# Performance work log

Hardware: AMD Instinct MI355X
Metric: run time of the kernel (lower is better)

Reference implementation:

```python
import jax, jax.numpy as jnp
import numpy as np

B, S, H, D = 4, 4096, 8, 128
EPS = 1e-6


def layernorm(x, g, b, axes):
    m = jnp.mean(x, axis=axes, keepdims=True)
    v = jnp.mean(jnp.square(x - m), axis=axes, keepdims=True)
    return (x - m) / jnp.sqrt(v + EPS) * g + b


def setup_inputs() -> dict:
    key = jax.random.key(0)
    ks = jax.random.split(key, 6)
    scale = 0.05
    return {
        "heads_input": jax.random.normal(ks[0], (B, S, H, D), jnp.float32),
        # GroupLinear trans_hid: per-head (2D -> 3D)
        "W_hid": jax.random.normal(ks[1], (H, 2 * D, 3 * D), jnp.float32) * scale,
        "b_hid": jax.random.normal(ks[2], (H, 3 * D), jnp.float32) * scale,
        # GroupLinear trans_og: per-head (2D -> D)
        "W_og": jax.random.normal(ks[3], (H, 2 * D, D), jnp.float32) * scale,
        "b_og": jax.random.normal(ks[4], (H, D), jnp.float32) * scale,
        # LayerNorm affine params (elementwise_affine=True)
        "ln_csum_g": jnp.ones((H, D), jnp.float32),
        "ln_csum_b": jnp.zeros((H, D), jnp.float32),
        "ln_hid_g": jnp.ones((H, 3, D), jnp.float32),
        "ln_hid_b": jnp.zeros((H, 3, D), jnp.float32),
        "ln_og_g": jnp.ones((H, D), jnp.float32),
        "ln_og_b": jnp.zeros((H, D), jnp.float32),
        "init_cx": jnp.zeros((1, H, D), jnp.float32),
    }


def reference(heads_input, W_hid, b_hid, W_og, b_og, ln_csum_g, ln_csum_b,
              ln_hid_g, ln_hid_b, ln_og_g, ln_og_b, init_cx):
    b, s, h, d = heads_input.shape
    # shifted cumulative sum over time, then LayerNorm over (head, dim)
    shifted = jnp.concatenate(
        [jnp.zeros((b, 1, h, d), heads_input.dtype), heads_input[:, :-1]], axis=1)
    csum = layernorm(jnp.cumsum(shifted, axis=1), ln_csum_g, ln_csum_b, (-2, -1))
    cat = jnp.concatenate([heads_input, csum], axis=-1)        # [b,s,h,2d]
    hid = jnp.einsum('bshi,hio->bsho', cat, W_hid) + b_hid     # [b,s,h,3d]
    hid = layernorm(hid.reshape(b, s, h, 3, d), ln_hid_g, ln_hid_b, (-3, -2, -1))
    igate, fgate, hidden = hid[..., 0, :], hid[..., 1, :], hid[..., 2, :]
    fgate = jax.nn.sigmoid(fgate)
    igh = jax.nn.sigmoid(igate) * jax.nn.relu(hidden)
    # LGateFunc: cell_t = fgate_t * cell_{t-1} + igh_t, cell_0 = init_cx
    c0 = jnp.broadcast_to(init_cx, (b, h, d)).astype(heads_input.dtype)
    def step(c, fi):
        f, i = fi
        c = f * c + i
        return c, c
    _, cells = jax.lax.scan(step, c0,
                            (fgate.transpose(1, 0, 2, 3), igh.transpose(1, 0, 2, 3)))
    cell = cells.transpose(1, 0, 2, 3)                          # [b,s,h,d]
    og_in = jnp.concatenate([heads_input, cell], axis=-1)       # [b,s,h,2d]
    og = layernorm(jnp.einsum('bshi,hio->bsho', og_in, W_og) + b_og,
                   ln_og_g, ln_og_b, (-2, -1))
    return jax.nn.sigmoid(og) * cell
```

## Files before the change

### kernel.cpp

```cpp
#include <hip/hip_runtime.h>

#define EPSF 1e-6f


typedef __attribute__((ext_vector_type(8))) short short8v;
typedef __attribute__((ext_vector_type(4))) float float4v;

__device__ __forceinline__ float sigm(float x) { return 1.0f / (1.0f + __expf(-x)); }

__device__ __forceinline__ unsigned short f2bf(float f) {
    unsigned int u = __float_as_uint(f);
    u = (u + 0x7fffu + ((u >> 16) & 1u)) >> 16;
    return (unsigned short)u;
}
__device__ __forceinline__ float bf2f(unsigned short s) { return __uint_as_float(((unsigned int)s) << 16); }
__device__ __forceinline__ float bf2f_lo(unsigned int p) { return __uint_as_float(p << 16); }
__device__ __forceinline__ float bf2f_hi(unsigned int p) { return __uint_as_float(p & 0xffff0000u); }
__device__ __forceinline__ unsigned int pack2bf(float a, float b) {
    return (unsigned int)f2bf(a) | ((unsigned int)f2bf(b) << 16);
}

__device__ __forceinline__ void block_reduce2(float& a, float& b) {
#pragma unroll
    for (int off = 32; off > 0; off >>= 1) {
        a += __shfl_down(a, off);
        b += __shfl_down(b, off);
    }
    __shared__ float sa[8], sb[8];
    int wid = threadIdx.x >> 6;
    int lane = threadIdx.x & 63;
    if (lane == 0) { sa[wid] = a; sb[wid] = b; }
    __syncthreads();
    a = sa[0] + sa[1] + sa[2] + sa[3];
    b = sb[0] + sb[1] + sb[2] + sb[3];
}

__global__ __launch_bounds__(256) void k_prep_w(const float* __restrict__ W, unsigned short* __restrict__ Wt,
                                                int Nw) {
    int idx = blockIdx.x * 256 + threadIdx.x;
    int k = idx & 255;
    int rest = idx >> 8;
    int o = rest % Nw;
    int h = rest / Nw;
    Wt[idx] = f2bf(W[((size_t)h * 256 + k) * Nw + o]);
}

__global__ __launch_bounds__(256) void k_cumsum_a(const float* __restrict__ X, float* __restrict__ cS,
                                                  unsigned short* __restrict__ XB) {
    int t = blockIdx.x * 256 + threadIdx.x;
    int d = t & 127, h = (t >> 7) & 7, k = (t >> 10) & 63, b = t >> 16;
    size_t base = (((size_t)(b * 4096 + k * 64)) * 8 + h) * 128 + d;
    float s = 0.f;
    for (int j = 0; j < 64; ++j) {
        unsigned short xb = f2bf(X[base + (size_t)j * 1024]);
        XB[base + (size_t)j * 1024] = xb;
        s += bf2f(xb);
    }
    cS[(size_t)((b * 8 + h) * 128 + d) * 64 + k] = s;
}

__global__ __launch_bounds__(256) void k_cumsum_b(const float* __restrict__ cS, float* __restrict__ cO) {
    int ch = blockIdx.x * 256 + threadIdx.x;
    size_t base = (size_t)ch * 64;
    float off = 0.f;
    for (int k = 0; k < 64; ++k) { float v = cS[base + k]; cO[base + k] = off; off += v; }
}

__global__ __launch_bounds__(256) void k_cumsum_c(const unsigned short* __restrict__ XB,
                                                  const float* __restrict__ cO,
                                                  unsigned short* __restrict__ CSUMB) {
    int t = blockIdx.x * 256 + threadIdx.x;
    int d = t & 127, h = (t >> 7) & 7, k = (t >> 10) & 63, b = t >> 16;
    int ch = (b * 8 + h) * 128 + d;
    float run = cO[(size_t)ch * 64 + k];
    size_t base = (((size_t)(b * 4096 + k * 64)) * 8 + h) * 128 + d;
    for (int j = 0; j < 64; ++j) {
        float x = bf2f(XB[base + (size_t)j * 1024]);
        CSUMB[base + (size_t)j * 1024] = f2bf(run);
        run += x;
    }
}

__global__ __launch_bounds__(256) void k_ln_csum(const unsigned short* __restrict__ CSUMB,
                                                 unsigned short* __restrict__ CSB,
                                                 const float* __restrict__ g, const float* __restrict__ bb) {
    int bs = blockIdx.x, t = threadIdx.x;
    uint2 u = ((const uint2*)(CSUMB + (size_t)bs * 1024))[t];
    float4 v;
    v.x = bf2f_lo(u.x); v.y = bf2f_hi(u.x);
    v.z = bf2f_lo(u.y); v.w = bf2f_hi(u.y);
    float s = v.x + v.y + v.z + v.w;
    float ss = v.x * v.x + v.y * v.y + v.z * v.z + v.w * v.w;
    block_reduce2(s, ss);
    float m = s * (1.f / 1024.f);
    float var = ss * (1.f / 1024.f) - m * m;
    float r = rsqrtf(fmaxf(var, 0.f) + EPSF);
    float4 gv = ((const float4*)g)[t];
    float4 bv = ((const float4*)bb)[t];
    uint2 o;
    o.x = pack2bf((v.x - m) * r * gv.x + bv.x, (v.y - m) * r * gv.y + bv.y);
    o.y = pack2bf((v.z - m) * r * gv.z + bv.z, (v.w - m) * r * gv.w + bv.w);
    ((uint2*)(CSB + (size_t)bs * 1024))[t] = o;
}

__global__ __launch_bounds__(256) void k_gemm_bf16(const unsigned short* __restrict__ A1,
                                                   const unsigned short* __restrict__ A2,
                                                   const unsigned short* __restrict__ Wt,
                                                   const float* __restrict__ bias,
                                                   unsigned short* __restrict__ OUT, int Nw, int m0) {
    __shared__ short As[16384];
    __shared__ short Bs[16384];
    int h = blockIdx.z, by = blockIdx.y, bx = blockIdx.x;
    int t = threadIdx.x;
    int lane = t & 63, wid = t >> 6;
    int wr = wid >> 1, wc = wid & 1;
    int l15 = lane & 15, l4 = lane >> 4;
    float4v acc[4][4];
#pragma unroll
    for (int i = 0; i < 4; ++i)
#pragma unroll
        for (int j = 0; j < 4; ++j) acc[i][j] = (float4v)(0.f);

    const size_t mbase = (size_t)(m0 + by * 128);
    for (int ks = 0; ks < 2; ++ks) {
        const unsigned short* Asrc = ks ? A2 : A1;
#pragma unroll
        for (int it = 0; it < 8; ++it) {
            int r0 = wid * 32 + it * 4;
            int r = r0 + l4;
            size_t g = ((mbase + r) * 8 + h) * 128 + 8 * (l15 ^ (r & 7));
            __builtin_amdgcn_global_load_lds((const __attribute__((address_space(1))) void*)(Asrc + g),
                                             (__attribute__((address_space(3))) void*)(As + r0 * 128),
                                             16, 0, 0);
        }
#pragma unroll
        for (int it = 0; it < 8; ++it) {
            int n0 = wid * 32 + it * 4;
            int nl = n0 + l4;
            size_t g = ((size_t)(h * Nw + bx * 128 + nl)) * 256 + ks * 128 + 8 * (l15 ^ (nl & 7));
            __builtin_amdgcn_global_load_lds((const __attribute__((address_space(1))) void*)(Wt + g),
                                             (__attribute__((address_space(3))) void*)(Bs + n0 * 128),
                                             16, 0, 0);
        }
        asm volatile("s_waitcnt vmcnt(0)" ::: "memory");
        __syncthreads();
#pragma unroll
        for (int kk = 0; kk < 4; ++kk) {
            short8v a[4], b[4];
#pragma unroll
            for (int i = 0; i < 4; ++i) {
                int r = wr * 64 + i * 16 + l15;
                int slot = (kk * 4 + l4) ^ (r & 7);
                a[i] = *(const short8v*)(As + r * 128 + slot * 8);
            }
#pragma unroll
            for (int j = 0; j < 4; ++j) {
                int c = wc * 64 + j * 16 + l15;
                int slot = (kk * 4 + l4) ^ (c & 7);
                b[j] = *(const short8v*)(Bs + c * 128 + slot * 8);
            }
#pragma unroll
            for (int i = 0; i < 4; ++i)
#pragma unroll
                for (int j = 0; j < 4; ++j)
                    acc[i][j] = __builtin_amdgcn_mfma_f32_16x16x32_bf16(a[i], b[j], acc[i][j], 0, 0, 0);
        }
        __syncthreads();
    }
#pragma unroll
    for (int j = 0; j < 4; ++j) {
        int o = bx * 128 + wc * 64 + j * 16 + l15;
        float bv = bias[h * Nw + o];
#pragma unroll
        for (int i = 0; i < 4; ++i) {
            int mlb = by * 128 + wr * 64 + i * 16 + l4 * 4;
#pragma unroll
            for (int q = 0; q < 4; ++q) {
                OUT[((size_t)(mlb + q) * 8 + h) * Nw + o] = f2bf(acc[i][j][q] + bv);
            }
        }
    }
}

__global__ __launch_bounds__(256) void k_ln_gates(const unsigned short* __restrict__ HID,
                                                  unsigned short* __restrict__ FG,
                                                  unsigned short* __restrict__ IG,
                                                  const float* __restrict__ g, const float* __restrict__ bb,
                                                  int m0) {
    __shared__ float sm[3072];
    int bsl = blockIdx.x, t = threadIdx.x;
    int bs = m0 + bsl;
    const uint4* row = (const uint4*)(HID + (size_t)bsl * 3072);
    float s = 0.f, ss = 0.f;
    for (int idx = t; idx < 384; idx += 256) {
        uint4 u = row[idx];
        float f0 = bf2f_lo(u.x), f1 = bf2f_hi(u.x);
        float f2 = bf2f_lo(u.y), f3 = bf2f_hi(u.y);
        float f4 = bf2f_lo(u.z), f5 = bf2f_hi(u.z);
        float f6 = bf2f_lo(u.w), f7 = bf2f_hi(u.w);
        float* p = sm + idx * 8;
        p[0] = f0; p[1] = f1; p[2] = f2; p[3] = f3; p[4] = f4; p[5] = f5; p[6] = f6; p[7] = f7;
        s += f0 + f1 + f2 + f3 + f4 + f5 + f6 + f7;
        ss += f0 * f0 + f1 * f1 + f2 * f2 + f3 * f3 + f4 * f4 + f5 * f5 + f6 * f6 + f7 * f7;
    }
    block_reduce2(s, ss);
    float m = s * (1.f / 3072.f);
    float var = ss * (1.f / 3072.f) - m * m;
    float r = rsqrtf(fmaxf(var, 0.f) + EPSF);
    int u0 = t * 4;
    int h = u0 >> 7;
    int d0 = u0 & 127;
    float fr[4], ir[4];
#pragma unroll
    for (int q = 0; q < 4; ++q) {
        int d = d0 + q;
        float yi = sm[h * 384 + d];
        float yf = sm[h * 384 + 128 + d];
        float yh = sm[h * 384 + 256 + d];
        float ni = (yi - m) * r * g[(h * 3 + 0) * 128 + d] + bb[(h * 3 + 0) * 128 + d];
        float nf = (yf - m) * r * g[(h * 3 + 1) * 128 + d] + bb[(h * 3 + 1) * 128 + d];
        float nh = (yh - m) * r * g[(h * 3 + 2) * 128 + d] + bb[(h * 3 + 2) * 128 + d];
        fr[q] = sigm(nf);
        ir[q] = sigm(ni) * fmaxf(nh, 0.f);
    }
    uint2 fo, io;
    fo.x = pack2bf(fr[0], fr[1]); fo.y = pack2bf(fr[2], fr[3]);
    io.x = pack2bf(ir[0], ir[1]); io.y = pack2bf(ir[2], ir[3]);
    ((uint2*)(FG + (size_t)bs * 1024))[t] = fo;
    ((uint2*)(IG + (size_t)bs * 1024))[t] = io;
}

__global__ __launch_bounds__(256) void k_scan_a(const unsigned short* __restrict__ FG,
                                                const unsigned short* __restrict__ IG,
                                                float* __restrict__ cF, float* __restrict__ cC) {
    int t = blockIdx.x * 256 + threadIdx.x;
    int d2 = t & 63, h = (t >> 6) & 7, k = (t >> 9) & 63, b = t >> 15;
    size_t base = (((size_t)(b * 4096 + k * 64)) * 8 + h) * 64 + d2;
    const unsigned int* FGu = (const unsigned int*)FG;
    const unsigned int* IGu = (const unsigned int*)IG;
    float F0 = 1.f, C0 = 0.f, F1 = 1.f, C1 = 0.f;
    for (int j = 0; j < 64; ++j) {
        unsigned int fg = FGu[base + (size_t)j * 512];
        unsigned int ig = IGu[base + (size_t)j * 512];
        float f0 = bf2f_lo(fg), f1 = bf2f_hi(fg);
        C0 = fmaf(f0, C0, bf2f_lo(ig)); F0 *= f0;
        C1 = fmaf(f1, C1, bf2f_hi(ig)); F1 *= f1;
    }
    size_t ci0 = ((size_t)((b * 8 + h) * 128 + d2 * 2)) * 64 + k;
    cF[ci0] = F0; cC[ci0] = C0;
    cF[ci0 + 64] = F1; cC[ci0 + 64] = C1;
}

__global__ __launch_bounds__(256) void k_scan_b(const float* __restrict__ cF, const float* __restrict__ cC,
                                                const float* __restrict__ initcx, float* __restrict__ cI) {
    int ch = blockIdx.x * 256 + threadIdx.x;
    float c = initcx[ch & 1023];
    size_t base = (size_t)ch * 64;
    for (int k = 0; k < 64; ++k) {
        cI[base + k] = c;
        c = fmaf(cF[base + k], c, cC[base + k]);
    }
}

__global__ __launch_bounds__(256) void k_scan_c(const unsigned short* __restrict__ FG,
                                                unsigned short* __restrict__ IGCLB,
                                                const float* __restrict__ cI) {
    int t = blockIdx.x * 256 + threadIdx.x;
    int d2 = t & 63, h = (t >> 6) & 7, k = (t >> 9) & 63, b = t >> 15;
    size_t base = (((size_t)(b * 4096 + k * 64)) * 8 + h) * 64 + d2;
    const unsigned int* FGu = (const unsigned int*)FG;
    unsigned int* IGu = (unsigned int*)IGCLB;
    size_t ci0 = ((size_t)((b * 8 + h) * 128 + d2 * 2)) * 64 + k;
    float c0 = cI[ci0], c1 = cI[ci0 + 64];
    for (int j = 0; j < 64; ++j) {
        unsigned int fg = FGu[base + (size_t)j * 512];
        unsigned int ig = IGu[base + (size_t)j * 512];
        c0 = fmaf(bf2f_lo(fg), c0, bf2f_lo(ig));
        c1 = fmaf(bf2f_hi(fg), c1, bf2f_hi(ig));
        IGu[base + (size_t)j * 512] = pack2bf(c0, c1);
    }
}

__global__ __launch_bounds__(256) void k_ln_out(const unsigned short* __restrict__ OG,
                                                const unsigned short* __restrict__ CLB,
                                                const float* __restrict__ g, const float* __restrict__ bb,
                                                float* __restrict__ OUT, int m0) {
    int bsl = blockIdx.x, t = threadIdx.x;
    int bs = m0 + bsl;
    uint2 u = ((const uint2*)(OG + (size_t)bsl * 1024))[t];
    float4 v;
    v.x = bf2f_lo(u.x); v.y = bf2f_hi(u.x);
    v.z = bf2f_lo(u.y); v.w = bf2f_hi(u.y);
    float s = v.x + v.y + v.z + v.w;
    float ss = v.x * v.x + v.y * v.y + v.z * v.z + v.w * v.w;
    block_reduce2(s, ss);
    float m = s * (1.f / 1024.f);
    float var = ss * (1.f / 1024.f) - m * m;
    float r = rsqrtf(fmaxf(var, 0.f) + EPSF);
    float4 gv = ((const float4*)g)[t];
    float4 bv = ((const float4*)bb)[t];
    uint2 cu = ((const uint2*)(CLB + (size_t)bs * 1024))[t];
    float4 cv;
    cv.x = bf2f_lo(cu.x); cv.y = bf2f_hi(cu.x);
    cv.z = bf2f_lo(cu.y); cv.w = bf2f_hi(cu.y);
    float4 o;
    o.x = sigm((v.x - m) * r * gv.x + bv.x) * cv.x;
    o.y = sigm((v.y - m) * r * gv.y + bv.y) * cv.y;
    o.z = sigm((v.z - m) * r * gv.z + bv.z) * cv.z;
    o.w = sigm((v.w - m) * r * gv.w + bv.w) * cv.w;
    ((float4*)(OUT + (size_t)bs * 1024))[t] = o;
}

extern "C" void kernel_launch(void* const* d_in, const int* in_sizes, int n_in,
                              void* d_out, int out_size, void* d_ws, size_t ws_size,
                              hipStream_t stream) {
    const float* X      = (const float*)d_in[0];
    const float* W_hid  = (const float*)d_in[1];
    const float* b_hid  = (const float*)d_in[2];
    const float* W_og   = (const float*)d_in[3];
    const float* b_og   = (const float*)d_in[4];
    const float* g_cs   = (const float*)d_in[5];
    const float* b_cs   = (const float*)d_in[6];
    const float* g_hid  = (const float*)d_in[7];
    const float* b_hidl = (const float*)d_in[8];
    const float* g_og   = (const float*)d_in[9];
    const float* b_ogl  = (const float*)d_in[10];
    const float* initcx = (const float*)d_in[11];

    float* ws = (float*)d_ws;
    const size_t O_SC    = 0ull;
    const size_t O_XB    = 1310720ull;
    const size_t O_CSUMB = 9699328ull;
    const size_t O_CSB   = 18087936ull;
    const size_t O_IGB   = 26476544ull;
    const size_t O_WTH   = 34865152ull;
    const size_t O_WTO   = 35258368ull;
    const size_t O_HID   = 35389440ull;

    float* cS = ws + O_SC;
    float* cO = cS + 262144;
    float* cF = cO + 262144;
    float* cC = cF + 262144;
    float* cI = cC + 262144;
    unsigned short* XB    = (unsigned short*)(ws + O_XB);
    unsigned short* CSUMB = (unsigned short*)(ws + O_CSUMB);
    unsigned short* FGB   = CSUMB;
    unsigned short* CSB   = (unsigned short*)(ws + O_CSB);
    unsigned short* IGB   = (unsigned short*)(ws + O_IGB);
    unsigned short* CLB   = IGB;
    unsigned short* WTH   = (unsigned short*)(ws + O_WTH);
    unsigned short* WTO   = (unsigned short*)(ws + O_WTO);
    unsigned short* HIDC  = (unsigned short*)(ws + O_HID);

    size_t avail = (ws_size / 4 > O_HID) ? ws_size / 4 - O_HID : 0;
    int CH = 1024;
    for (int c = 16384; c >= 1024; c >>= 1) {
        if ((size_t)c * 1536ull <= avail) { CH = c; break; }
    }
    const int NC = 16384 / CH;

    dim3 blk(256);
    k_prep_w<<<3072, blk, 0, stream>>>(W_hid, WTH, 384);
    k_prep_w<<<1024, blk, 0, stream>>>(W_og, WTO, 128);
    k_cumsum_a<<<1024, blk, 0, stream>>>(X, cS, XB);
    k_cumsum_b<<<16, blk, 0, stream>>>(cS, cO);
    k_cumsum_c<<<1024, blk, 0, stream>>>(XB, cO, CSUMB);
    k_ln_csum<<<16384, blk, 0, stream>>>(CSUMB, CSB, g_cs, b_cs);
    for (int c = 0; c < NC; ++c) {
        int m0 = c * CH;
        k_gemm_bf16<<<dim3(3, CH / 128, 8), blk, 0, stream>>>(XB, CSB, WTH, b_hid, HIDC, 384, m0);
        k_ln_gates<<<CH, blk, 0, stream>>>(HIDC, FGB, IGB, g_hid, b_hidl, m0);
    }
    k_scan_a<<<512, blk, 0, stream>>>(FGB, IGB, cF, cC);
    k_scan_b<<<16, blk, 0, stream>>>(cF, cC, initcx, cI);
    k_scan_c<<<512, blk, 0, stream>>>(FGB, IGB, cI);
    for (int c = 0; c < NC; ++c) {
        int m0 = c * CH;
        k_gemm_bf16<<<dim3(1, CH / 128, 8), blk, 0, stream>>>(XB, CLB, WTO, b_og, HIDC, 128, m0);
        k_ln_out<<<CH, blk, 0, stream>>>(HIDC, CLB, g_og, b_ogl, (float*)d_out, m0);
    }
}
```

Baseline: 257.5 us.

## Double-buffer GEMM K-tiles in LDS and remap grid with head-fastest block order

The bf16 GEMM now splits the K dimension into four 64-wide stages and double-buffers them in LDS, so the next stage's global-to-LDS load overlaps the MFMA work on the current one, using partial vmcnt waits and raw barriers. The launch grid is flattened to 1D with the head index fastest, so adjacent blocks work on different heads of the same rows. This keeps the same LDS footprint but adds more barriers and finer-grained stages, and it relies on the vmcnt(8) count matching the number of loads issued per stage.

```diff
diff --git a/kernel.cpp b/kernel.cpp
--- a/kernel.cpp
+++ b/kernel.cpp
@@ -107,57 +107,77 @@
                                                    const unsigned short* __restrict__ A2,
                                                    const unsigned short* __restrict__ Wt,
                                                    const float* __restrict__ bias,
-                                                   unsigned short* __restrict__ OUT, int Nw, int m0) {
-    __shared__ short As[16384];
-    __shared__ short Bs[16384];
-    int h = blockIdx.z, by = blockIdx.y, bx = blockIdx.x;
-    int t = threadIdx.x;
-    int lane = t & 63, wid = t >> 6;
+                                                   unsigned short* __restrict__ OUT, int Nw, int m0,
+                                                   int nbx) {
+    __shared__ short As[2][8192];
+    __shared__ short Bs[2][8192];
+    int bid = blockIdx.x;
+    int h = bid & 7;
+    int rest = bid >> 3;
+    int bx = rest % nbx;
+    int by = rest / nbx;
+    int t0 = threadIdx.x;
+    int lane = t0 & 63, wid = t0 >> 6;
     int wr = wid >> 1, wc = wid & 1;
     int l15 = lane & 15, l4 = lane >> 4;
+    int lr = lane >> 3, lc = lane & 7;
+    const int bxc = bx * 128;
+    const size_t mbase = (size_t)(m0 + by * 128);
+
     float4v acc[4][4];
 #pragma unroll
     for (int i = 0; i < 4; ++i)
 #pragma unroll
         for (int j = 0; j < 4; ++j) acc[i][j] = (float4v)(0.f);
 
-    const size_t mbase = (size_t)(m0 + by * 128);
-    for (int ks = 0; ks < 2; ++ks) {
-        const unsigned short* Asrc = ks ? A2 : A1;
-#pragma unroll
-        for (int it = 0; it < 8; ++it) {
-            int r0 = wid * 32 + it * 4;
-            int r = r0 + l4;
-            size_t g = ((mbase + r) * 8 + h) * 128 + 8 * (l15 ^ (r & 7));
-            __builtin_amdgcn_global_load_lds((const __attribute__((address_space(1))) void*)(Asrc + g),
-                                             (__attribute__((address_space(3))) void*)(As + r0 * 128),
+    auto STAGE = [&](int t, int buf) {
+        const unsigned short* src = (t < 2) ? A1 : A2;
+        int kofs = (t & 1) * 64;
+#pragma unroll
+        for (int it = 0; it < 4; ++it) {
+            int r0 = wid * 32 + it * 8;
+            int r = r0 + lr;
+            int c = lc ^ (r & 7);
+            size_t g = ((mbase + r) * 8 + h) * 128 + kofs + c * 8;
+            __builtin_amdgcn_global_load_lds((const __attribute__((address_space(1))) void*)(src + g),
+                                             (__attribute__((address_space(3))) void*)(&As[buf][r0 * 64]),
                                              16, 0, 0);
         }
 #pragma unroll
-        for (int it = 0; it < 8; ++it) {
-            int n0 = wid * 32 + it * 4;
-            int nl = n0 + l4;
-            size_t g = ((size_t)(h * Nw + bx * 128 + nl)) * 256 + ks * 128 + 8 * (l15 ^ (nl & 7));
+        for (int it = 0; it < 4; ++it) {
+            int n0 = wid * 32 + it * 8;
+            int cl = n0 + lr;
+            int c = lc ^ (cl & 7);
+            size_t g = ((size_t)(h * Nw + bxc + cl)) * 256 + t * 64 + c * 8;
             __builtin_amdgcn_global_load_lds((const __attribute__((address_space(1))) void*)(Wt + g),
-                                             (__attribute__((address_space(3))) void*)(Bs + n0 * 128),
+                                             (__attribute__((address_space(3))) void*)(&Bs[buf][n0 * 64]),
                                              16, 0, 0);
         }
-        asm volatile("s_waitcnt vmcnt(0)" ::: "memory");
-        __syncthreads();
-#pragma unroll
-        for (int kk = 0; kk < 4; ++kk) {
+    };
+
+    STAGE(0, 0);
+#pragma unroll
+    for (int t = 0; t < 4; ++t) {
+        int cur = t & 1;
+        if (t < 3) STAGE(t + 1, cur ^ 1);
+        if (t < 3) asm volatile("s_waitcnt vmcnt(8)" ::: "memory");
+        else       asm volatile("s_waitcnt vmcnt(0)" ::: "memory");
+        __builtin_amdgcn_s_barrier();
+        __builtin_amdgcn_sched_barrier(0);
+#pragma unroll
+        for (int kk = 0; kk < 2; ++kk) {
             short8v a[4], b[4];
 #pragma unroll
             for (int i = 0; i < 4; ++i) {
                 int r = wr * 64 + i * 16 + l15;
                 int slot = (kk * 4 + l4) ^ (r & 7);
-                a[i] = *(const short8v*)(As + r * 128 + slot * 8);
+                a[i] = *(const short8v*)(&As[cur][r * 64 + slot * 8]);
             }
 #pragma unroll
             for (int j = 0; j < 4; ++j) {
                 int c = wc * 64 + j * 16 + l15;
                 int slot = (kk * 4 + l4) ^ (c & 7);
-                b[j] = *(const short8v*)(Bs + c * 128 + slot * 8);
+                b[j] = *(const short8v*)(&Bs[cur][c * 64 + slot * 8]);
             }
 #pragma unroll
             for (int i = 0; i < 4; ++i)
@@ -165,11 +185,12 @@
                 for (int j = 0; j < 4; ++j)
                     acc[i][j] = __builtin_amdgcn_mfma_f32_16x16x32_bf16(a[i], b[j], acc[i][j], 0, 0, 0);
         }
-        __syncthreads();
+        __builtin_amdgcn_sched_barrier(0);
+        __builtin_amdgcn_s_barrier();
     }
 #pragma unroll
     for (int j = 0; j < 4; ++j) {
-        int o = bx * 128 + wc * 64 + j * 16 + l15;
+        int o = bxc + wc * 64 + j * 16 + l15;
         float bv = bias[h * Nw + o];
 #pragma unroll
         for (int i = 0; i < 4; ++i) {
@@ -368,7 +389,7 @@
     k_ln_csum<<<16384, blk, 0, stream>>>(CSUMB, CSB, g_cs, b_cs);
     for (int c = 0; c < NC; ++c) {
         int m0 = c * CH;
-        k_gemm_bf16<<<dim3(3, CH / 128, 8), blk, 0, stream>>>(XB, CSB, WTH, b_hid, HIDC, 384, m0);
+        k_gemm_bf16<<<8 * 3 * (CH / 128), blk, 0, stream>>>(XB, CSB, WTH, b_hid, HIDC, 384, m0, 3);
         k_ln_gates<<<CH, blk, 0, stream>>>(HIDC, FGB, IGB, g_hid, b_hidl, m0);
     }
     k_scan_a<<<512, blk, 0, stream>>>(FGB, IGB, cF, cC);
@@ -376,7 +397,7 @@
     k_scan_c<<<512, blk, 0, stream>>>(FGB, IGB, cI);
     for (int c = 0; c < NC; ++c) {
         int m0 = c * CH;
-        k_gemm_bf16<<<dim3(1, CH / 128, 8), blk, 0, stream>>>(XB, CLB, WTO, b_og, HIDC, 128, m0);
+        k_gemm_bf16<<<8 * 1 * (CH / 128), blk, 0, stream>>>(XB, CLB, WTO, b_og, HIDC, 128, m0, 1);
         k_ln_out<<<CH, blk, 0, stream>>>(HIDC, CLB, g_og, b_ogl, (float*)d_out, m0);
     }
 }
```

After: 242.0 us. -6.0%, faster.
